# Performance work log

Measured on AMD Instinct MI355X. Metric: run time of the kernel, lower is better.

Reference implementation:

```python
import jax, jax.numpy as jnp
import numpy as np

SAMPLE_RATE = 44100
LOWEST_HZ = 55.0
L_ORDER = 5
NUM_COEFF = L_ORDER + 1          # 6 loop-filter coefficients
NUM_ACTIVE = NUM_COEFF + 1       # 7 taps for linear interpolation
VEC_SIZE = int(SAMPLE_RATE // LOWEST_HZ) + NUM_ACTIVE  # 808 = LPC order
N_FRAMES = 128
N_SAMPLES = 65536


def _natural_cubic_spline(y, t_out):
    """Natural cubic spline through y[n, d] at uniform knots on [0,1], eval at t_out[T]."""
    n, d = y.shape
    h = 1.0 / (n - 1)
    # second derivatives M with natural BC (M0 = Mn-1 = 0): tridiag solve
    rhs = 6.0 * (y[2:] - 2.0 * y[1:-1] + y[:-2]) / (h * h)          # [n-2, d]
    T = 4.0 * jnp.eye(n - 2, dtype=y.dtype) \
        + jnp.eye(n - 2, k=1, dtype=y.dtype) + jnp.eye(n - 2, k=-1, dtype=y.dtype)
    M_inner = jnp.linalg.solve(T, rhs)
    zero = jnp.zeros((1, d), y.dtype)
    M = jnp.concatenate([zero, M_inner, zero], axis=0)              # [n, d]
    idx = jnp.clip(jnp.floor(t_out * (n - 1)).astype(jnp.int32), 0, n - 2)
    s = (t_out - idx.astype(y.dtype) * h)[:, None]                  # [T, 1]
    yi, yi1, Mi, Mi1 = y[idx], y[idx + 1], M[idx], M[idx + 1]
    b = (yi1 - yi) / h - h * (2.0 * Mi + Mi1) / 6.0
    return yi + b * s + 0.5 * Mi * s * s + (Mi1 - Mi) * (s ** 3) / (6.0 * h)


def setup_inputs() -> dict:
    key = jax.random.key(0)
    k1, k2, k3 = jax.random.split(key, 3)
    # delay in samples, in [100, 300) so floor(delay)+6 < VEC_SIZE always
    delay_len_frames = 100.0 + 200.0 * jax.random.uniform(k1, (N_FRAMES,), dtype=jnp.float32)
    raw_gain = jnp.zeros((), jnp.float32)  # nn.Parameter init 0.0
    # raw (pre-sigmoid) coefficients, uniform in coeff_range = (-2, 0)
    raw_coeff_frames = jax.random.uniform(k2, (N_FRAMES, NUM_COEFF), dtype=jnp.float32,
                                          minval=-2.0, maxval=0.0)
    exc_coefficients = jnp.zeros((1, N_SAMPLES, 1), jnp.float32)  # zeros init, order 1
    burst = jax.random.normal(k3, (N_SAMPLES,), jnp.float32)      # excitation noise burst
    return {"delay_len_frames": delay_len_frames, "raw_gain": raw_gain,
            "raw_coeff_frames": raw_coeff_frames, "exc_coefficients": exc_coefficients,
            "burst": burst, "n_samples": N_SAMPLES}


def _forward(delay_len_frames, raw_gain, raw_coeff_frames, exc_coefficients, burst, n_samples):
    dtype = jnp.float32
    # get_constrained_coefficients: sigmoid -> normalize to sum 1 -> scale by gain
    sig = jax.nn.sigmoid(raw_coeff_frames)
    coeff_frames = sig / sig.sum(-1, keepdims=True) * jax.nn.sigmoid(raw_gain)  # [F, 6]
    # get_upsampled_parameters: natural cubic spline from n_frames -> n_samples
    t_out = jnp.linspace(0.0, 1.0, n_samples, dtype=dtype)
    delay_i = _natural_cubic_spline(delay_len_frames[:, None].astype(dtype), t_out)[:, 0]  # [T]
    b = _natural_cubic_spline(coeff_frames.astype(dtype), t_out)                           # [T, 6]
    # linear fractional-delay taps: z_l..z_l+6 (floor->int breaks grad, alfa keeps it)
    z_l = jnp.floor(delay_i).astype(jnp.int32)
    alfa = (delay_i - z_l.astype(dtype))[:, None]
    # A[t, z_l+i] values (sparse representation of the [T, VEC_SIZE] tap matrix)
    vals = -jnp.concatenate([(1.0 - alfa) * b[:, :1],
                             alfa * b[:, :-1] + (1.0 - alfa) * b[:, 1:],
                             alfa * b[:, -1:]], axis=1)                                    # [T, 7]
    # excitation LPC (order 1, time-varying): x[t] = burst[t] - a[t]*x[t-1]
    a1 = exc_coefficients[0, :, 0]
    def exc_step(ym1, inp):
        xt, at = inp
        y = xt - at * ym1
        return y, y
    _, x = jax.lax.scan(exc_step, jnp.zeros((), dtype), (burst.astype(dtype), a1))
    # Karplus-Strong recursion: y[t] = x[t] - sum_j A[t,j]*y[t-1-j]; buf[j] = y[t-1-j]
    def ks_step(buf, inp):
        xt, v, z = inp
        taps = jax.lax.dynamic_slice(buf, (z,), (NUM_ACTIVE,))
        y = xt - jnp.dot(v, taps)
        buf = jnp.concatenate([y[None], buf[:-1]])
        return buf, y
    buf0 = jnp.zeros((VEC_SIZE,), dtype)
    _, y_out = jax.lax.scan(ks_step, buf0, (x, vals, z_l))
    return y_out


def reference(delay_len_frames, raw_gain, raw_coeff_frames, exc_coefficients, burst, n_samples):
    return _forward(delay_len_frames, raw_gain, raw_coeff_frames,
                    exc_coefficients, burst, n_samples)
```

## Files before the change

kernel.cpp:

```cpp
#include <hip/hip_runtime.h>
#include <math.h>
#include <limits.h>

#define N_SAMPLES 65536
#define N_FRAMES  128
#define NUM_COEFF 6
#define NSEG      126
#define VEC_SIZE  808
#define ZCLAMP    (VEC_SIZE - 7)

#define WS_XL    0
#define WS_PP    262144
#define WS_VALS  524288
#define WS_TM    2621440
#define WS_TC    2621696
#define WS_D     2621952
#define WS_PL    2622464
#define WS_MQ    5768192

struct CpTab { double v[NSEG]; };
static constexpr CpTab make_cp() {
    CpTab t{};
    t.v[0] = 0.25;
    for (int i = 1; i < NSEG; ++i) t.v[i] = 1.0 / (4.0 - t.v[i - 1]);
    return t;
}
__device__ __constant__ CpTab CP = make_cp();

__global__ __launch_bounds__(256) void k_front(
    const float* __restrict__ delay_len,
    const float* __restrict__ raw_gain,
    const float* __restrict__ raw_coeff,
    const float* __restrict__ exc,
    const float* __restrict__ burst,
    float* __restrict__ ws)
{
    const int tid = threadIdx.x;
    const int b = blockIdx.x;

    if (b >= 256) {
        float* xl = ws + WS_XL / 4;
        float* PP = ws + WS_PP / 4;
        float* TM = ws + WS_TM / 4;
        float* TC = ws + WS_TC / 4;
        const int tile = b - 256;
        const int base = tile * 1024 + tid * 4;

        if (tile == 0 && tid == 0) *(int*)((char*)ws + WS_D) = 0x7fffffff;

        const float4 a4 = *(const float4*)(exc + base);
        const float4 b4 = *(const float4*)(burst + base);

        float m = -a4.x,            c = b4.x;
        m = -a4.y * m;              c = b4.y - a4.y * c;
        m = -a4.z * m;              c = b4.z - a4.z * c;
        m = -a4.w * m;              c = b4.w - a4.w * c;

        __shared__ float sm[256], sc[256];
        sm[tid] = m; sc[tid] = c;
        __syncthreads();
        for (int off = 1; off < 256; off <<= 1) {
            const float cm = sm[tid], cc = sc[tid];
            float pm = 1.f, pc = 0.f;
            if (tid >= off) { pm = sm[tid - off]; pc = sc[tid - off]; }
            __syncthreads();
            if (tid >= off) { sm[tid] = cm * pm; sc[tid] = cm * pc + cc; }
            __syncthreads();
        }
        float y = (tid == 0) ? 0.f : sc[tid - 1];
        float P = (tid == 0) ? 1.f : sm[tid - 1];

        float4 x4, p4;
        y = b4.x - a4.x * y;  P = -a4.x * P;  x4.x = y; p4.x = P;
        y = b4.y - a4.y * y;  P = -a4.y * P;  x4.y = y; p4.y = P;
        y = b4.z - a4.z * y;  P = -a4.z * P;  x4.z = y; p4.z = P;
        y = b4.w - a4.w * y;  P = -a4.w * P;  x4.w = y; p4.w = P;

        *(float4*)(xl + base) = x4;
        *(float4*)(PP + base) = p4;
        if (tid == 255) { TM[tile] = sm[255]; TC[tile] = sc[255]; }
        return;
    }

    float* vals8 = ws + WS_VALS / 4;
    __shared__ float Y[7][N_FRAMES];
    __shared__ float M[7][N_FRAMES];
    __shared__ double dp[7][NSEG];

    if (tid < N_FRAMES) {
        float s[NUM_COEFF];
        float sum = 0.f;
        for (int j = 0; j < NUM_COEFF; ++j) {
            s[j] = 1.f / (1.f + expf(-raw_coeff[tid * NUM_COEFF + j]));
            sum += s[j];
        }
        const float gain = 1.f / (1.f + expf(-raw_gain[0]));
        for (int j = 0; j < NUM_COEFF; ++j)
            Y[1 + j][tid] = s[j] / sum * gain;
        Y[0][tid] = delay_len[tid];
    }
    __syncthreads();

    if (tid < 7) {
        const float* y = Y[tid];
        const double inv_h2 = 127.0 * 127.0;
        double prev = 6.0 * ((double)y[2] - 2.0 * (double)y[1] + (double)y[0]) * inv_h2 * 0.25;
        dp[tid][0] = prev;
        for (int i = 1; i < NSEG; ++i) {
            double ri = 6.0 * ((double)y[i + 2] - 2.0 * (double)y[i + 1] + (double)y[i]) * inv_h2;
            prev = (ri - prev) * CP.v[i];
            dp[tid][i] = prev;
        }
        float* Mc = M[tid];
        Mc[0] = 0.f; Mc[N_FRAMES - 1] = 0.f;
        double mi = dp[tid][NSEG - 1];
        Mc[NSEG] = (float)mi;
        for (int i = NSEG - 2; i >= 0; --i) {
            mi = dp[tid][i] - CP.v[i] * mi;
            Mc[i + 1] = (float)mi;
        }
    }
    __syncthreads();

    const int t = b * 256 + tid;
    const float h = 1.0f / 127.0f;
    const float tf = (float)t * (1.0f / 65535.0f);
    int idx = (int)floorf(tf * 127.0f);
    idx = min(max(idx, 0), 126);
    const float s = tf - (float)idx * h;
    const float s2 = s * s;
    const float s3 = s2 * s;

    float o[7];
#pragma unroll
    for (int c = 0; c < 7; ++c) {
        const float yi  = Y[c][idx];
        const float yi1 = Y[c][idx + 1];
        const float Mi  = M[c][idx];
        const float Mi1 = M[c][idx + 1];
        const float bb = (yi1 - yi) / h - h * (2.f * Mi + Mi1) / 6.f;
        o[c] = yi + bb * s + 0.5f * Mi * s2 + (Mi1 - Mi) * s3 / (6.f * h);
    }
    const float delay = o[0];
    int z = (int)floorf(delay);
    const float alfa = delay - (float)z;
    z = min(max(z, 0), ZCLAMP);

    float v[8];
    v[0] = -((1.f - alfa) * o[1]);
#pragma unroll
    for (int j = 1; j <= 5; ++j)
        v[j] = -(alfa * o[j] + (1.f - alfa) * o[j + 1]);
    v[6] = -(alfa * o[6]);
    v[7] = (float)z;

    float4* vp = (float4*)(vals8 + (size_t)t * 8);
    vp[0] = make_float4(v[0], v[1], v[2], v[3]);
    vp[1] = make_float4(v[4], v[5], v[6], v[7]);
}

__device__ __forceinline__ unsigned int bf16_hi(float f) {
    unsigned int b = __float_as_uint(f);
    b = b + 0x7fffu + ((b >> 16) & 1u);
    return b & 0xffff0000u;
}
__device__ __forceinline__ unsigned int bf16_lo(float f) {
    unsigned int b = __float_as_uint(f);
    b = b + 0x7fffu + ((b >> 16) & 1u);
    return b >> 16;
}

__global__ __launch_bounds__(256) void k_exp(float* __restrict__ ws)
{
    __shared__ float accL[256 * 33];
    __shared__ float xwin[1920];
    __shared__ float yin[64];
    __shared__ int dmin;
    const int tid = threadIdx.x;
    const int T0 = blockIdx.x * 256;
    const int t = T0 + tid;
    const int wlo = T0 - 1664;

    const float* xl = ws + WS_XL / 4;
    const float* PP = ws + WS_PP / 4;
    const float* vals8 = ws + WS_VALS / 4;
    const float* TM = ws + WS_TM / 4;
    const float* TC = ws + WS_TC / 4;
    float4* PL = (float4*)((char*)ws + WS_PL);
    float4* MQ = (float4*)((char*)ws + WS_MQ);
    int* D = (int*)((char*)ws + WS_D);

    float* acc = accL + tid * 33;
#pragma unroll
    for (int o = 0; o < 32; ++o) acc[o] = 0.f;

    if (tid == 0) dmin = 0x7fffffff;
    if (tid < 64) {
        float m = TM[tid], c = TC[tid];
#pragma unroll
        for (int off = 1; off < 64; off <<= 1) {
            const float pm = __shfl_up(m, off, 64);
            const float pc = __shfl_up(c, off, 64);
            if (tid >= off) { c = fmaf(m, pc, c); m *= pm; }
        }
        const float yp = __shfl_up(c, 1, 64);
        yin[tid] = (tid == 0) ? 0.f : yp;
    }
    __syncthreads();

    for (int i = tid; i < 1920; i += 256) {
        const int p = wlo + i;
        float xv = 0.f;
        if (p >= 0 && p < N_SAMPLES)
            xv = xl[p] + PP[p] * yin[p >> 10];
        xwin[i] = xv;
    }
    __syncthreads();

#define XREAD(p) xwin[(p) - wlo]

    const float4* vp = (const float4*)(vals8 + (size_t)t * 8);
    const float4 r0 = vp[0], r1 = vp[1];
    const float vj[7] = {r0.x, r0.y, r0.z, r0.w, r1.x, r1.y, r1.z};
    const int m0 = t - 1 - (int)r1.w;
    float X1 = XREAD(t);

    float4 s0[7], s1[7];
    float xs[7];
    int sm0[7];
    bool val[7];
    int pmin = INT_MAX;
#pragma unroll
    for (int j = 0; j < 7; ++j) {
        const int s = m0 - j;
        val[j] = (s >= 0);
        const int si = val[j] ? s : 0;
        const float4* sp = (const float4*)(vals8 + (size_t)si * 8);
        s0[j] = sp[0]; s1[j] = sp[1];
        xs[j] = XREAD(val[j] ? s : t);
        sm0[j] = s - 1 - (int)s1[j].w;
        if (val[j]) pmin = min(pmin, sm0[j]);
    }
    if (pmin == INT_MAX) pmin = t - 900;
    const int B1 = (pmin - 6) & ~3;

#pragma unroll
    for (int j = 0; j < 7; ++j) {
        if (!val[j]) continue;
        X1 -= vj[j] * xs[j];
        const float sv[7] = {s0[j].x, s0[j].y, s0[j].z, s0[j].w,
                             s1[j].x, s1[j].y, s1[j].z};
        const int ob = sm0[j] - B1;
#pragma unroll
        for (int k = 0; k < 7; ++k) {
            int o = ob - k;
            o = min(max(o, 0), 31);
            acc[o] += vj[j] * sv[k];
        }
    }

    float c1f[32];
#pragma unroll
    for (int o = 0; o < 32; ++o) { c1f[o] = acc[o]; acc[o] = 0.f; }

    float X15 = X1;
    int first = -1;
#pragma unroll
    for (int o = 0; o < 32; ++o)
        if (first < 0 && c1f[o] != 0.f && (B1 + o) >= 0) first = o;

    int B2 = 0, maxq = INT_MIN;
    if (first >= 0) {
        const int pf = B1 + first;
        const float zf = ((const float4*)(vals8 + (size_t)pf * 8))[1].w;
        B2 = ((pf - 1 - (int)zf) - 6) & ~3;

#pragma unroll
        for (int o = 0; o < 32; ++o) {
            const float co = c1f[o];
            const int p = B1 + o;
            if (co == 0.f || p < 0) continue;
            const float4* pv = (const float4*)(vals8 + (size_t)p * 8);
            const float4 v0 = pv[0], v1 = pv[1];
            X15 += co * XREAD(p);
            const int rp = p - 1 - (int)v1.w;
            maxq = max(maxq, rp);
            const float sv[7] = {v0.x, v0.y, v0.z, v0.w, v1.x, v1.y, v1.z};
            const int ob = rp - B2;
#pragma unroll
            for (int j = 0; j < 7; ++j) {
                int oo = ob - j;
                oo = min(max(oo, 0), 27);
                acc[oo] -= co * sv[j];
            }
        }
    }
#undef XREAD

    unsigned int u[14];
#pragma unroll
    for (int i = 0; i < 14; ++i)
        u[i] = bf16_lo(acc[2 * i]) | (bf16_lo(acc[2 * i + 1]) << 16);

    PL[t]             = make_float4(__uint_as_float(u[0]),  __uint_as_float(u[1]),
                                    __uint_as_float(u[2]),  __uint_as_float(u[3]));
    PL[t + 65536]     = make_float4(__uint_as_float(u[4]),  __uint_as_float(u[5]),
                                    __uint_as_float(u[6]),  __uint_as_float(u[7]));
    PL[t + 2 * 65536] = make_float4(__uint_as_float(u[8]),  __uint_as_float(u[9]),
                                    __uint_as_float(u[10]), __uint_as_float(u[11]));
    MQ[t] = make_float4(X15, (float)(B2 & 2047),
                        __uint_as_float(u[12]), __uint_as_float(u[13]));

    if (first >= 0 && maxq > INT_MIN) atomicMin(&dmin, t - maxq);
    __syncthreads();
    if (tid == 0) atomicMin(D, dmin);
}

__device__ __forceinline__ void bar_lgkm() {
    asm volatile("s_waitcnt lgkmcnt(0)\n\ts_barrier" ::: "memory");
}

typedef float f32x4 __attribute__((ext_vector_type(4)));

#define GLD4(dst, p)                                                           \
    asm volatile("global_load_dwordx4 %0, %1, off" : "=v"(dst) : "v"(p))

#define VWAIT8(a, b, c, d)                                                     \
    asm volatile("s_waitcnt vmcnt(8)"                                          \
        : "+v"(a), "+v"(b), "+v"(c), "+v"(d))

#define DOT2BF(acc_, a_, b_)                                                   \
    asm("v_dot2_f32_bf16 %0, %1, %2, %0" : "+v"(acc_) : "v"(a_), "v"(b_))

__global__ __launch_bounds__(320, 1) void k_ks3(
    const float* __restrict__ ws_c,
    float* __restrict__ out)
{
    __shared__ __align__(16) unsigned short ringb[4096];
    const int tid = threadIdx.x;
    const f32x4* PL = (const f32x4*)((const char*)ws_c + WS_PL);
    const f32x4* MQ = (const f32x4*)((const char*)ws_c + WS_MQ);
    const int* Dp = (const int*)((const char*)ws_c + WS_D);

    for (int i = tid; i < 4096; i += 320) ringb[i] = 0;
    __syncthreads();

    int C = *Dp;
    if (C > 320) C = 320;
    if (C < 1) C = 1;
    const int C3 = 3 * C;

#define PRE(P0, P1, P2, PM, BASE)                                              \
    do {                                                                       \
        int tL = (BASE) + tid; if (tL > N_SAMPLES - 1) tL = N_SAMPLES - 1;     \
        GLD4(P0, PL + tL);             GLD4(P1, PL + tL + 65536);              \
        GLD4(P2, PL + tL + 2 * 65536); GLD4(PM, MQ + tL);                      \
    } while (0)

#define DOT(P0, P1, P2, PM, YOUT)                                              \
    do {                                                                       \
        const int idx_ = (int)(PM).y;                                          \
        const unsigned int u_[14] = {                                          \
            __float_as_uint((P0).x), __float_as_uint((P0).y),                  \
            __float_as_uint((P0).z), __float_as_uint((P0).w),                  \
            __float_as_uint((P1).x), __float_as_uint((P1).y),                  \
            __float_as_uint((P1).z), __float_as_uint((P1).w),                  \
            __float_as_uint((P2).x), __float_as_uint((P2).y),                  \
            __float_as_uint((P2).z), __float_as_uint((P2).w),                  \
            __float_as_uint((PM).z), __float_as_uint((PM).w)};                 \
        float p0 = 0.f, p1 = 0.f;                                              \
        _Pragma("unroll")                                                      \
        for (int q = 0; q < 7; ++q) {                                          \
            const uint2 rr_ = *(const uint2*)&ringb[idx_ + 4 * q];             \
            DOT2BF(p0, u_[2 * q],     rr_.x);                                  \
            DOT2BF(p1, u_[2 * q + 1], rr_.y);                                  \
        }                                                                      \
        YOUT = (PM).x + (p0 + p1);                                             \
    } while (0)

#define STEP(P0, P1, P2, PM, S_)                                               \
    do {                                                                       \
        VWAIT8(P0, P1, P2, PM);                                                \
        const int t0 = (S_) + tid;                                             \
        if (tid < C && t0 < N_SAMPLES) {                                       \
            float y0; DOT(P0, P1, P2, PM, y0);                                 \
            const int w = t0 & 2047;                                           \
            const unsigned short yb = (unsigned short)bf16_lo(y0);             \
            ringb[w] = yb; ringb[w + 2048] = yb; out[t0] = y0;                 \
        }                                                                      \
        PRE(P0, P1, P2, PM, (S_) + C3);                                        \
        bar_lgkm();                                                            \
    } while (0)

    f32x4 A0, A1, A2, AM;
    f32x4 B0, B1, B2, BM;
    f32x4 U0, U1, U2, UM;

    PRE(A0, A1, A2, AM, 0);
    PRE(B0, B1, B2, BM, C);
    PRE(U0, U1, U2, UM, 2 * C);
    for (int S = 0; S < N_SAMPLES; S += C3) {
        STEP(A0, A1, A2, AM, S);
        STEP(B0, B1, B2, BM, S + C);
        STEP(U0, U1, U2, UM, S + 2 * C);
    }
#undef STEP
#undef DOT
#undef PRE
}

extern "C" void kernel_launch(void* const* d_in, const int* in_sizes, int n_in,
                              void* d_out, int out_size, void* d_ws, size_t ws_size,
                              hipStream_t stream)
{
    const float* delay_len = (const float*)d_in[0];
    const float* raw_gain  = (const float*)d_in[1];
    const float* raw_coeff = (const float*)d_in[2];
    const float* exc       = (const float*)d_in[3];
    const float* burst     = (const float*)d_in[4];
    float* ws  = (float*)d_ws;
    float* out = (float*)d_out;

    hipLaunchKernelGGL(k_front, dim3(320), dim3(256), 0, stream,
                       delay_len, raw_gain, raw_coeff, exc, burst, ws);
    hipLaunchKernelGGL(k_exp, dim3(256), dim3(256), 0, stream, ws);
    hipLaunchKernelGGL(k_ks3, dim3(1), dim3(320), 0, stream, ws, out);
}
```

Baseline: 162.5 us.

## Fuse three kernels into one cooperative kernel with grid syncs

Merges the front (IIR scan plus spline), expansion and sequential Karplus-Strong kernels into a single cooperative launch of 256 blocks of 320 threads, with grid.sync between phases and a shared-memory union. The aim is to remove two kernel launch and drain gaps. In exchange, every block in the earlier phases runs at 320 threads with idle lanes, and the cooperative launch and grid barriers add their own overhead. The serial final phase still runs on a single block.

```diff
diff --git a/kernel.cpp b/kernel.cpp
--- a/kernel.cpp
+++ b/kernel.cpp
@@ -1,6 +1,9 @@
 #include <hip/hip_runtime.h>
+#include <hip/hip_cooperative_groups.h>
 #include <math.h>
 #include <limits.h>
+
+namespace cg = cooperative_groups;
 
 #define N_SAMPLES 65536
 #define N_FRAMES  128
@@ -27,65 +30,105 @@
 }
 __device__ __constant__ CpTab CP = make_cp();
 
-__global__ __launch_bounds__(256) void k_front(
+__device__ __forceinline__ unsigned int bf16_hi(float f) {
+    unsigned int b = __float_as_uint(f);
+    b = b + 0x7fffu + ((b >> 16) & 1u);
+    return b & 0xffff0000u;
+}
+__device__ __forceinline__ unsigned int bf16_lo(float f) {
+    unsigned int b = __float_as_uint(f);
+    b = b + 0x7fffu + ((b >> 16) & 1u);
+    return b >> 16;
+}
+
+__device__ __forceinline__ void bar_lgkm() {
+    asm volatile("s_waitcnt lgkmcnt(0)\n\ts_barrier" ::: "memory");
+}
+
+typedef float f32x4 __attribute__((ext_vector_type(4)));
+
+#define GLD4(dst, p)                                                           \
+    asm volatile("global_load_dwordx4 %0, %1, off" : "=v"(dst) : "v"(p))
+
+#define VWAIT8(a, b, c, d)                                                     \
+    asm volatile("s_waitcnt vmcnt(8)"                                          \
+        : "+v"(a), "+v"(b), "+v"(c), "+v"(d))
+
+#define DOT2BF(acc_, a_, b_)                                                   \
+    asm("v_dot2_f32_bf16 %0, %1, %2, %0" : "+v"(acc_) : "v"(a_), "v"(b_))
+
+union SMemU {
+    struct { float sm[256]; float sc[256]; } iir;
+    struct { float Y[7][N_FRAMES]; float M[7][N_FRAMES]; double dp[7][NSEG]; } spl;
+    struct { float accL[256 * 33]; float xwin[1920]; float yin[64]; int dmin; } ex;
+    struct { unsigned short ringb[4096]; } ks;
+};
+
+__global__ __launch_bounds__(320, 1) void k_fused(
     const float* __restrict__ delay_len,
     const float* __restrict__ raw_gain,
     const float* __restrict__ raw_coeff,
     const float* __restrict__ exc,
     const float* __restrict__ burst,
-    float* __restrict__ ws)
+    float* __restrict__ ws,
+    float* __restrict__ out)
 {
+    __shared__ __align__(16) SMemU smem;
     const int tid = threadIdx.x;
     const int b = blockIdx.x;
-
-    if (b >= 256) {
-        float* xl = ws + WS_XL / 4;
-        float* PP = ws + WS_PP / 4;
-        float* TM = ws + WS_TM / 4;
-        float* TC = ws + WS_TC / 4;
-        const int tile = b - 256;
-        const int base = tile * 1024 + tid * 4;
-
-        if (tile == 0 && tid == 0) *(int*)((char*)ws + WS_D) = 0x7fffffff;
-
-        const float4 a4 = *(const float4*)(exc + base);
-        const float4 b4 = *(const float4*)(burst + base);
-
-        float m = -a4.x,            c = b4.x;
-        m = -a4.y * m;              c = b4.y - a4.y * c;
-        m = -a4.z * m;              c = b4.z - a4.z * c;
-        m = -a4.w * m;              c = b4.w - a4.w * c;
-
-        __shared__ float sm[256], sc[256];
-        sm[tid] = m; sc[tid] = c;
+    cg::grid_group grid = cg::this_grid();
+
+    float* xl = ws + WS_XL / 4;
+    float* PP = ws + WS_PP / 4;
+    float* TM = ws + WS_TM / 4;
+    float* TC = ws + WS_TC / 4;
+    float* vals8 = ws + WS_VALS / 4;
+    int* D = (int*)((char*)ws + WS_D);
+
+    if (b == 0 && tid == 0) *D = 0x7fffffff;
+
+    if (b < 64) {
+        const int base = b * 1024 + tid * 4;
+        float4 a4, b4;
+        if (tid < 256) {
+            a4 = *(const float4*)(exc + base);
+            b4 = *(const float4*)(burst + base);
+
+            float m = -a4.x,            c = b4.x;
+            m = -a4.y * m;              c = b4.y - a4.y * c;
+            m = -a4.z * m;              c = b4.z - a4.z * c;
+            m = -a4.w * m;              c = b4.w - a4.w * c;
+            smem.iir.sm[tid] = m; smem.iir.sc[tid] = c;
+        }
         __syncthreads();
         for (int off = 1; off < 256; off <<= 1) {
-            const float cm = sm[tid], cc = sc[tid];
-            float pm = 1.f, pc = 0.f;
-            if (tid >= off) { pm = sm[tid - off]; pc = sc[tid - off]; }
+            float cm = 0.f, cc = 0.f, pm = 1.f, pc = 0.f;
+            if (tid < 256) {
+                cm = smem.iir.sm[tid]; cc = smem.iir.sc[tid];
+                if (tid >= off) { pm = smem.iir.sm[tid - off]; pc = smem.iir.sc[tid - off]; }
+            }
             __syncthreads();
-            if (tid >= off) { sm[tid] = cm * pm; sc[tid] = cm * pc + cc; }
+            if (tid < 256 && tid >= off) {
+                smem.iir.sm[tid] = cm * pm; smem.iir.sc[tid] = cm * pc + cc;
+            }
             __syncthreads();
         }
-        float y = (tid == 0) ? 0.f : sc[tid - 1];
-        float P = (tid == 0) ? 1.f : sm[tid - 1];
-
-        float4 x4, p4;
-        y = b4.x - a4.x * y;  P = -a4.x * P;  x4.x = y; p4.x = P;
-        y = b4.y - a4.y * y;  P = -a4.y * P;  x4.y = y; p4.y = P;
-        y = b4.z - a4.z * y;  P = -a4.z * P;  x4.z = y; p4.z = P;
-        y = b4.w - a4.w * y;  P = -a4.w * P;  x4.w = y; p4.w = P;
-
-        *(float4*)(xl + base) = x4;
-        *(float4*)(PP + base) = p4;
-        if (tid == 255) { TM[tile] = sm[255]; TC[tile] = sc[255]; }
-        return;
-    }
-
-    float* vals8 = ws + WS_VALS / 4;
-    __shared__ float Y[7][N_FRAMES];
-    __shared__ float M[7][N_FRAMES];
-    __shared__ double dp[7][NSEG];
+        if (tid < 256) {
+            float y = (tid == 0) ? 0.f : smem.iir.sc[tid - 1];
+            float P = (tid == 0) ? 1.f : smem.iir.sm[tid - 1];
+
+            float4 x4, p4;
+            y = b4.x - a4.x * y;  P = -a4.x * P;  x4.x = y; p4.x = P;
+            y = b4.y - a4.y * y;  P = -a4.y * P;  x4.y = y; p4.y = P;
+            y = b4.z - a4.z * y;  P = -a4.z * P;  x4.z = y; p4.z = P;
+            y = b4.w - a4.w * y;  P = -a4.w * P;  x4.w = y; p4.w = P;
+
+            *(float4*)(xl + base) = x4;
+            *(float4*)(PP + base) = p4;
+            if (tid == 255) { TM[b] = smem.iir.sm[255]; TC[b] = smem.iir.sc[255]; }
+        }
+        __syncthreads();
+    }
 
     if (tid < N_FRAMES) {
         float s[NUM_COEFF];
@@ -96,265 +139,232 @@
         }
         const float gain = 1.f / (1.f + expf(-raw_gain[0]));
         for (int j = 0; j < NUM_COEFF; ++j)
-            Y[1 + j][tid] = s[j] / sum * gain;
-        Y[0][tid] = delay_len[tid];
+            smem.spl.Y[1 + j][tid] = s[j] / sum * gain;
+        smem.spl.Y[0][tid] = delay_len[tid];
     }
     __syncthreads();
 
     if (tid < 7) {
-        const float* y = Y[tid];
+        const float* y = smem.spl.Y[tid];
         const double inv_h2 = 127.0 * 127.0;
         double prev = 6.0 * ((double)y[2] - 2.0 * (double)y[1] + (double)y[0]) * inv_h2 * 0.25;
-        dp[tid][0] = prev;
+        smem.spl.dp[tid][0] = prev;
         for (int i = 1; i < NSEG; ++i) {
             double ri = 6.0 * ((double)y[i + 2] - 2.0 * (double)y[i + 1] + (double)y[i]) * inv_h2;
             prev = (ri - prev) * CP.v[i];
-            dp[tid][i] = prev;
-        }
-        float* Mc = M[tid];
+            smem.spl.dp[tid][i] = prev;
+        }
+        float* Mc = smem.spl.M[tid];
         Mc[0] = 0.f; Mc[N_FRAMES - 1] = 0.f;
-        double mi = dp[tid][NSEG - 1];
+        double mi = smem.spl.dp[tid][NSEG - 1];
         Mc[NSEG] = (float)mi;
         for (int i = NSEG - 2; i >= 0; --i) {
-            mi = dp[tid][i] - CP.v[i] * mi;
+            mi = smem.spl.dp[tid][i] - CP.v[i] * mi;
             Mc[i + 1] = (float)mi;
         }
     }
     __syncthreads();
 
-    const int t = b * 256 + tid;
-    const float h = 1.0f / 127.0f;
-    const float tf = (float)t * (1.0f / 65535.0f);
-    int idx = (int)floorf(tf * 127.0f);
-    idx = min(max(idx, 0), 126);
-    const float s = tf - (float)idx * h;
-    const float s2 = s * s;
-    const float s3 = s2 * s;
-
-    float o[7];
-#pragma unroll
-    for (int c = 0; c < 7; ++c) {
-        const float yi  = Y[c][idx];
-        const float yi1 = Y[c][idx + 1];
-        const float Mi  = M[c][idx];
-        const float Mi1 = M[c][idx + 1];
-        const float bb = (yi1 - yi) / h - h * (2.f * Mi + Mi1) / 6.f;
-        o[c] = yi + bb * s + 0.5f * Mi * s2 + (Mi1 - Mi) * s3 / (6.f * h);
-    }
-    const float delay = o[0];
-    int z = (int)floorf(delay);
-    const float alfa = delay - (float)z;
-    z = min(max(z, 0), ZCLAMP);
-
-    float v[8];
-    v[0] = -((1.f - alfa) * o[1]);
-#pragma unroll
-    for (int j = 1; j <= 5; ++j)
-        v[j] = -(alfa * o[j] + (1.f - alfa) * o[j + 1]);
-    v[6] = -(alfa * o[6]);
-    v[7] = (float)z;
-
-    float4* vp = (float4*)(vals8 + (size_t)t * 8);
-    vp[0] = make_float4(v[0], v[1], v[2], v[3]);
-    vp[1] = make_float4(v[4], v[5], v[6], v[7]);
-}
-
-__device__ __forceinline__ unsigned int bf16_hi(float f) {
-    unsigned int b = __float_as_uint(f);
-    b = b + 0x7fffu + ((b >> 16) & 1u);
-    return b & 0xffff0000u;
-}
-__device__ __forceinline__ unsigned int bf16_lo(float f) {
-    unsigned int b = __float_as_uint(f);
-    b = b + 0x7fffu + ((b >> 16) & 1u);
-    return b >> 16;
-}
-
-__global__ __launch_bounds__(256) void k_exp(float* __restrict__ ws)
-{
-    __shared__ float accL[256 * 33];
-    __shared__ float xwin[1920];
-    __shared__ float yin[64];
-    __shared__ int dmin;
-    const int tid = threadIdx.x;
-    const int T0 = blockIdx.x * 256;
-    const int t = T0 + tid;
-    const int wlo = T0 - 1664;
-
-    const float* xl = ws + WS_XL / 4;
-    const float* PP = ws + WS_PP / 4;
-    const float* vals8 = ws + WS_VALS / 4;
-    const float* TM = ws + WS_TM / 4;
-    const float* TC = ws + WS_TC / 4;
-    float4* PL = (float4*)((char*)ws + WS_PL);
-    float4* MQ = (float4*)((char*)ws + WS_MQ);
-    int* D = (int*)((char*)ws + WS_D);
-
-    float* acc = accL + tid * 33;
-#pragma unroll
-    for (int o = 0; o < 32; ++o) acc[o] = 0.f;
-
-    if (tid == 0) dmin = 0x7fffffff;
-    if (tid < 64) {
-        float m = TM[tid], c = TC[tid];
-#pragma unroll
-        for (int off = 1; off < 64; off <<= 1) {
-            const float pm = __shfl_up(m, off, 64);
-            const float pc = __shfl_up(c, off, 64);
-            if (tid >= off) { c = fmaf(m, pc, c); m *= pm; }
-        }
-        const float yp = __shfl_up(c, 1, 64);
-        yin[tid] = (tid == 0) ? 0.f : yp;
-    }
-    __syncthreads();
-
-    for (int i = tid; i < 1920; i += 256) {
-        const int p = wlo + i;
-        float xv = 0.f;
-        if (p >= 0 && p < N_SAMPLES)
-            xv = xl[p] + PP[p] * yin[p >> 10];
-        xwin[i] = xv;
-    }
-    __syncthreads();
-
-#define XREAD(p) xwin[(p) - wlo]
-
-    const float4* vp = (const float4*)(vals8 + (size_t)t * 8);
-    const float4 r0 = vp[0], r1 = vp[1];
-    const float vj[7] = {r0.x, r0.y, r0.z, r0.w, r1.x, r1.y, r1.z};
-    const int m0 = t - 1 - (int)r1.w;
-    float X1 = XREAD(t);
-
-    float4 s0[7], s1[7];
-    float xs[7];
-    int sm0[7];
-    bool val[7];
-    int pmin = INT_MAX;
-#pragma unroll
-    for (int j = 0; j < 7; ++j) {
-        const int s = m0 - j;
-        val[j] = (s >= 0);
-        const int si = val[j] ? s : 0;
-        const float4* sp = (const float4*)(vals8 + (size_t)si * 8);
-        s0[j] = sp[0]; s1[j] = sp[1];
-        xs[j] = XREAD(val[j] ? s : t);
-        sm0[j] = s - 1 - (int)s1[j].w;
-        if (val[j]) pmin = min(pmin, sm0[j]);
-    }
-    if (pmin == INT_MAX) pmin = t - 900;
-    const int B1 = (pmin - 6) & ~3;
-
-#pragma unroll
-    for (int j = 0; j < 7; ++j) {
-        if (!val[j]) continue;
-        X1 -= vj[j] * xs[j];
-        const float sv[7] = {s0[j].x, s0[j].y, s0[j].z, s0[j].w,
-                             s1[j].x, s1[j].y, s1[j].z};
-        const int ob = sm0[j] - B1;
-#pragma unroll
-        for (int k = 0; k < 7; ++k) {
-            int o = ob - k;
-            o = min(max(o, 0), 31);
-            acc[o] += vj[j] * sv[k];
-        }
-    }
-
-    float c1f[32];
-#pragma unroll
-    for (int o = 0; o < 32; ++o) { c1f[o] = acc[o]; acc[o] = 0.f; }
-
-    float X15 = X1;
-    int first = -1;
-#pragma unroll
-    for (int o = 0; o < 32; ++o)
-        if (first < 0 && c1f[o] != 0.f && (B1 + o) >= 0) first = o;
-
-    int B2 = 0, maxq = INT_MIN;
-    if (first >= 0) {
-        const int pf = B1 + first;
-        const float zf = ((const float4*)(vals8 + (size_t)pf * 8))[1].w;
-        B2 = ((pf - 1 - (int)zf) - 6) & ~3;
-
-#pragma unroll
-        for (int o = 0; o < 32; ++o) {
-            const float co = c1f[o];
-            const int p = B1 + o;
-            if (co == 0.f || p < 0) continue;
-            const float4* pv = (const float4*)(vals8 + (size_t)p * 8);
-            const float4 v0 = pv[0], v1 = pv[1];
-            X15 += co * XREAD(p);
-            const int rp = p - 1 - (int)v1.w;
-            maxq = max(maxq, rp);
-            const float sv[7] = {v0.x, v0.y, v0.z, v0.w, v1.x, v1.y, v1.z};
-            const int ob = rp - B2;
+    if (tid < 256) {
+        const int t = b * 256 + tid;
+        const float h = 1.0f / 127.0f;
+        const float tf = (float)t * (1.0f / 65535.0f);
+        int idx = (int)floorf(tf * 127.0f);
+        idx = min(max(idx, 0), 126);
+        const float s = tf - (float)idx * h;
+        const float s2 = s * s;
+        const float s3 = s2 * s;
+
+        float o[7];
+#pragma unroll
+        for (int c = 0; c < 7; ++c) {
+            const float yi  = smem.spl.Y[c][idx];
+            const float yi1 = smem.spl.Y[c][idx + 1];
+            const float Mi  = smem.spl.M[c][idx];
+            const float Mi1 = smem.spl.M[c][idx + 1];
+            const float bb = (yi1 - yi) / h - h * (2.f * Mi + Mi1) / 6.f;
+            o[c] = yi + bb * s + 0.5f * Mi * s2 + (Mi1 - Mi) * s3 / (6.f * h);
+        }
+        const float delay = o[0];
+        int z = (int)floorf(delay);
+        const float alfa = delay - (float)z;
+        z = min(max(z, 0), ZCLAMP);
+
+        float v[8];
+        v[0] = -((1.f - alfa) * o[1]);
+#pragma unroll
+        for (int j = 1; j <= 5; ++j)
+            v[j] = -(alfa * o[j] + (1.f - alfa) * o[j + 1]);
+        v[6] = -(alfa * o[6]);
+        v[7] = (float)z;
+
+        float4* vp = (float4*)(vals8 + (size_t)t * 8);
+        vp[0] = make_float4(v[0], v[1], v[2], v[3]);
+        vp[1] = make_float4(v[4], v[5], v[6], v[7]);
+    }
+
+    __threadfence();
+    grid.sync();
+
+    {
+        float4* PL = (float4*)((char*)ws + WS_PL);
+        float4* MQ = (float4*)((char*)ws + WS_MQ);
+        const int T0 = b * 256;
+        const int t = T0 + tid;
+        const int wlo = T0 - 1664;
+
+        float* acc = smem.ex.accL + tid * 33;
+        if (tid < 256) {
+#pragma unroll
+            for (int o = 0; o < 32; ++o) acc[o] = 0.f;
+        }
+
+        if (tid == 0) smem.ex.dmin = 0x7fffffff;
+        if (tid < 64) {
+            float m = TM[tid], c = TC[tid];
+#pragma unroll
+            for (int off = 1; off < 64; off <<= 1) {
+                const float pm = __shfl_up(m, off, 64);
+                const float pc = __shfl_up(c, off, 64);
+                if (tid >= off) { c = fmaf(m, pc, c); m *= pm; }
+            }
+            const float yp = __shfl_up(c, 1, 64);
+            smem.ex.yin[tid] = (tid == 0) ? 0.f : yp;
+        }
+        __syncthreads();
+
+        for (int i = tid; i < 1920; i += 320) {
+            const int p = wlo + i;
+            float xv = 0.f;
+            if (p >= 0 && p < N_SAMPLES)
+                xv = xl[p] + PP[p] * smem.ex.yin[p >> 10];
+            smem.ex.xwin[i] = xv;
+        }
+        __syncthreads();
+
+        if (tid < 256) {
+#define XREAD(p) smem.ex.xwin[(p) - wlo]
+            const float4* vp = (const float4*)(vals8 + (size_t)t * 8);
+            const float4 r0 = vp[0], r1 = vp[1];
+            const float vj[7] = {r0.x, r0.y, r0.z, r0.w, r1.x, r1.y, r1.z};
+            const int m0 = t - 1 - (int)r1.w;
+            float X1 = XREAD(t);
+
+            float4 s0[7], s1[7];
+            float xs[7];
+            int sm0[7];
+            bool val[7];
+            int pmin = INT_MAX;
 #pragma unroll
             for (int j = 0; j < 7; ++j) {
-                int oo = ob - j;
-                oo = min(max(oo, 0), 27);
-                acc[oo] -= co * sv[j];
-            }
-        }
-    }
+                const int s = m0 - j;
+                val[j] = (s >= 0);
+                const int si = val[j] ? s : 0;
+                const float4* sp = (const float4*)(vals8 + (size_t)si * 8);
+                s0[j] = sp[0]; s1[j] = sp[1];
+                xs[j] = XREAD(val[j] ? s : t);
+                sm0[j] = s - 1 - (int)s1[j].w;
+                if (val[j]) pmin = min(pmin, sm0[j]);
+            }
+            if (pmin == INT_MAX) pmin = t - 900;
+            const int B1 = (pmin - 6) & ~3;
+
+#pragma unroll
+            for (int j = 0; j < 7; ++j) {
+                if (!val[j]) continue;
+                X1 -= vj[j] * xs[j];
+                const float sv[7] = {s0[j].x, s0[j].y, s0[j].z, s0[j].w,
+                                     s1[j].x, s1[j].y, s1[j].z};
+                const int ob = sm0[j] - B1;
+#pragma unroll
+                for (int k = 0; k < 7; ++k) {
+                    int o = ob - k;
+                    o = min(max(o, 0), 31);
+                    acc[o] += vj[j] * sv[k];
+                }
+            }
+
+            float c1f[32];
+#pragma unroll
+            for (int o = 0; o < 32; ++o) { c1f[o] = acc[o]; acc[o] = 0.f; }
+
+            float X15 = X1;
+            int first = -1;
+#pragma unroll
+            for (int o = 0; o < 32; ++o)
+                if (first < 0 && c1f[o] != 0.f && (B1 + o) >= 0) first = o;
+
+            int B2 = 0, maxq = INT_MIN;
+            if (first >= 0) {
+                const int pf = B1 + first;
+                const float zf = ((const float4*)(vals8 + (size_t)pf * 8))[1].w;
+                B2 = ((pf - 1 - (int)zf) - 6) & ~3;
+
+#pragma unroll
+                for (int o = 0; o < 32; ++o) {
+                    const float co = c1f[o];
+                    const int p = B1 + o;
+                    if (co == 0.f || p < 0) continue;
+                    const float4* pv = (const float4*)(vals8 + (size_t)p * 8);
+                    const float4 v0 = pv[0], v1 = pv[1];
+                    X15 += co * XREAD(p);
+                    const int rp = p - 1 - (int)v1.w;
+                    maxq = max(maxq, rp);
+                    const float sv[7] = {v0.x, v0.y, v0.z, v0.w, v1.x, v1.y, v1.z};
+                    const int ob = rp - B2;
+#pragma unroll
+                    for (int j = 0; j < 7; ++j) {
+                        int oo = ob - j;
+                        oo = min(max(oo, 0), 27);
+                        acc[oo] -= co * sv[j];
+                    }
+                }
+            }
 #undef XREAD
 
-    unsigned int u[14];
-#pragma unroll
-    for (int i = 0; i < 14; ++i)
-        u[i] = bf16_lo(acc[2 * i]) | (bf16_lo(acc[2 * i + 1]) << 16);
-
-    PL[t]             = make_float4(__uint_as_float(u[0]),  __uint_as_float(u[1]),
-                                    __uint_as_float(u[2]),  __uint_as_float(u[3]));
-    PL[t + 65536]     = make_float4(__uint_as_float(u[4]),  __uint_as_float(u[5]),
-                                    __uint_as_float(u[6]),  __uint_as_float(u[7]));
-    PL[t + 2 * 65536] = make_float4(__uint_as_float(u[8]),  __uint_as_float(u[9]),
-                                    __uint_as_float(u[10]), __uint_as_float(u[11]));
-    MQ[t] = make_float4(X15, (float)(B2 & 2047),
-                        __uint_as_float(u[12]), __uint_as_float(u[13]));
-
-    if (first >= 0 && maxq > INT_MIN) atomicMin(&dmin, t - maxq);
-    __syncthreads();
-    if (tid == 0) atomicMin(D, dmin);
-}
-
-__device__ __forceinline__ void bar_lgkm() {
-    asm volatile("s_waitcnt lgkmcnt(0)\n\ts_barrier" ::: "memory");
-}
-
-typedef float f32x4 __attribute__((ext_vector_type(4)));
-
-#define GLD4(dst, p)                                                           \
-    asm volatile("global_load_dwordx4 %0, %1, off" : "=v"(dst) : "v"(p))
-
-#define VWAIT8(a, b, c, d)                                                     \
-    asm volatile("s_waitcnt vmcnt(8)"                                          \
-        : "+v"(a), "+v"(b), "+v"(c), "+v"(d))
-
-#define DOT2BF(acc_, a_, b_)                                                   \
-    asm("v_dot2_f32_bf16 %0, %1, %2, %0" : "+v"(acc_) : "v"(a_), "v"(b_))
-
-__global__ __launch_bounds__(320, 1) void k_ks3(
-    const float* __restrict__ ws_c,
-    float* __restrict__ out)
-{
-    __shared__ __align__(16) unsigned short ringb[4096];
-    const int tid = threadIdx.x;
-    const f32x4* PL = (const f32x4*)((const char*)ws_c + WS_PL);
-    const f32x4* MQ = (const f32x4*)((const char*)ws_c + WS_MQ);
-    const int* Dp = (const int*)((const char*)ws_c + WS_D);
-
-    for (int i = tid; i < 4096; i += 320) ringb[i] = 0;
-    __syncthreads();
-
-    int C = *Dp;
-    if (C > 320) C = 320;
-    if (C < 1) C = 1;
-    const int C3 = 3 * C;
+            unsigned int u[14];
+#pragma unroll
+            for (int i = 0; i < 14; ++i)
+                u[i] = bf16_lo(acc[2 * i]) | (bf16_lo(acc[2 * i + 1]) << 16);
+
+            PL[t]             = make_float4(__uint_as_float(u[0]),  __uint_as_float(u[1]),
+                                            __uint_as_float(u[2]),  __uint_as_float(u[3]));
+            PL[t + 65536]     = make_float4(__uint_as_float(u[4]),  __uint_as_float(u[5]),
+                                            __uint_as_float(u[6]),  __uint_as_float(u[7]));
+            PL[t + 2 * 65536] = make_float4(__uint_as_float(u[8]),  __uint_as_float(u[9]),
+                                            __uint_as_float(u[10]), __uint_as_float(u[11]));
+            MQ[t] = make_float4(X15, (float)(B2 & 2047),
+                                __uint_as_float(u[12]), __uint_as_float(u[13]));
+
+            if (first >= 0 && maxq > INT_MIN) atomicMin(&smem.ex.dmin, t - maxq);
+        }
+        __syncthreads();
+        if (tid == 0) atomicMin(D, smem.ex.dmin);
+    }
+
+    __threadfence();
+    grid.sync();
+
+    if (b != 0) return;
+
+    {
+        unsigned short* ringb = smem.ks.ringb;
+        const f32x4* PLc = (const f32x4*)((const char*)ws + WS_PL);
+        const f32x4* MQc = (const f32x4*)((const char*)ws + WS_MQ);
+
+        for (int i = tid; i < 4096; i += 320) ringb[i] = 0;
+        __syncthreads();
+
+        int C = atomicMin(D, 0x7fffffff);
+        if (C > 320) C = 320;
+        if (C < 1) C = 1;
+        const int C3 = 3 * C;
 
 #define PRE(P0, P1, P2, PM, BASE)                                              \
     do {                                                                       \
         int tL = (BASE) + tid; if (tL > N_SAMPLES - 1) tL = N_SAMPLES - 1;     \
-        GLD4(P0, PL + tL);             GLD4(P1, PL + tL + 65536);              \
-        GLD4(P2, PL + tL + 2 * 65536); GLD4(PM, MQ + tL);                      \
+        GLD4(P0, PLc + tL);             GLD4(P1, PLc + tL + 65536);            \
+        GLD4(P2, PLc + tL + 2 * 65536); GLD4(PM, MQc + tL);                    \
     } while (0)
 
 #define DOT(P0, P1, P2, PM, YOUT)                                              \
@@ -392,21 +402,22 @@
         bar_lgkm();                                                            \
     } while (0)
 
-    f32x4 A0, A1, A2, AM;
-    f32x4 B0, B1, B2, BM;
-    f32x4 U0, U1, U2, UM;
-
-    PRE(A0, A1, A2, AM, 0);
-    PRE(B0, B1, B2, BM, C);
-    PRE(U0, U1, U2, UM, 2 * C);
-    for (int S = 0; S < N_SAMPLES; S += C3) {
-        STEP(A0, A1, A2, AM, S);
-        STEP(B0, B1, B2, BM, S + C);
-        STEP(U0, U1, U2, UM, S + 2 * C);
-    }
+        f32x4 A0, A1, A2, AM;
+        f32x4 B0, B1, B2, BM;
+        f32x4 U0, U1, U2, UM;
+
+        PRE(A0, A1, A2, AM, 0);
+        PRE(B0, B1, B2, BM, C);
+        PRE(U0, U1, U2, UM, 2 * C);
+        for (int S = 0; S < N_SAMPLES; S += C3) {
+            STEP(A0, A1, A2, AM, S);
+            STEP(B0, B1, B2, BM, S + C);
+            STEP(U0, U1, U2, UM, S + 2 * C);
+        }
 #undef STEP
 #undef DOT
 #undef PRE
+    }
 }
 
 extern "C" void kernel_launch(void* const* d_in, const int* in_sizes, int n_in,
@@ -421,8 +432,8 @@
     float* ws  = (float*)d_ws;
     float* out = (float*)d_out;
 
-    hipLaunchKernelGGL(k_front, dim3(320), dim3(256), 0, stream,
-                       delay_len, raw_gain, raw_coeff, exc, burst, ws);
-    hipLaunchKernelGGL(k_exp, dim3(256), dim3(256), 0, stream, ws);
-    hipLaunchKernelGGL(k_ks3, dim3(1), dim3(320), 0, stream, ws, out);
-}
+    void* args[] = { (void*)&delay_len, (void*)&raw_gain, (void*)&raw_coeff,
+                     (void*)&exc, (void*)&burst, (void*)&ws, (void*)&out };
+    hipLaunchCooperativeKernel((void*)k_fused, dim3(256), dim3(320),
+                               args, 0, stream);
+}
```

After: 288.6 us. 77.6% more time.
